# Kernel optimization log

Measured on AMD Instinct MI355X. Metric: run time of the kernel, lower is better.

The kernel has to match this reference:

```python
import jax, jax.numpy as jnp
import numpy as np

N_HEADS = 12
ROPE_THETA = 10000.0


def _rope(x):
    # x: [B, L, N, D]; interleaved (lucidrains rotary_embedding_torch style) rotation over full D
    B, L, N, D = x.shape
    inv_freq = 1.0 / (ROPE_THETA ** (jnp.arange(0, D, 2, dtype=jnp.float32) / D))  # [D/2]
    freqs = jnp.arange(L, dtype=jnp.float32)[:, None] * inv_freq                    # [L, D/2]
    cos = jnp.repeat(jnp.cos(freqs), 2, axis=-1)[None, :, None, :].astype(x.dtype)  # [1,L,1,D]
    sin = jnp.repeat(jnp.sin(freqs), 2, axis=-1)[None, :, None, :].astype(x.dtype)
    x1 = x[..., 0::2]
    x2 = x[..., 1::2]
    x_rot = jnp.stack([-x2, x1], axis=-1).reshape(x.shape)  # rotate_half, interleaved pairs
    return x * cos + x_rot * sin


def setup_inputs() -> dict:
    key = jax.random.key(0)
    ks = jax.random.split(key, 7)
    B, L, dm = 8, 1024, 768
    x = jax.random.normal(ks[0], (B, L, dm), jnp.float32)
    mask = jax.random.randint(ks[1], (B, L), 0, 2, jnp.int32)          # 1 = keep, 0 = pad
    pos_bias = jax.random.normal(ks[2], (N_HEADS, L, L), jnp.float32) * 0.1
    qkv_w = jax.random.normal(ks[3], (3 * dm, dm), jnp.float32) * 0.02
    qkv_b = jax.random.normal(ks[4], (3 * dm,), jnp.float32) * 0.02
    out_w = jax.random.normal(ks[5], (dm, dm), jnp.float32) * 0.02
    out_b = jax.random.normal(ks[6], (dm,), jnp.float32) * 0.02
    return {"x": x, "pos_bias": pos_bias, "qkv_w": qkv_w, "qkv_b": qkv_b,
            "out_w": out_w, "out_b": out_b, "mask": mask}


def reference(x, pos_bias, qkv_w, qkv_b, out_w, out_b, mask):
    B, L, dm = x.shape
    N = N_HEADS
    D = dm // N
    # QKV projection (torch Linear: y = x @ W.T + b), chunk(3, -1)
    qkv = x @ qkv_w.T + qkv_b                                   # [B, L, 3*dm]
    q, k, v = [a.reshape(B, L, N, D) for a in jnp.split(qkv, 3, axis=-1)]
    q = _rope(q)
    k = _rope(k)
    # scores [B, N, Lq, Lk]
    scores = jnp.einsum('bqnd,bknd->bnqk', q, k) / jnp.sqrt(jnp.asarray(D, x.dtype))
    # mask_to_bias: (mask - 1) with negatives -> -inf, shape [B, 1, 1, L]
    mask_bias = jnp.where(mask > 0, 0.0, -jnp.inf).astype(x.dtype)[:, None, None, :]
    bias = pos_bias[None].astype(x.dtype) + mask_bias           # [B, N, L, L]
    attn = jax.nn.softmax(scores + bias, axis=-1)               # dropout = 0 (eval)
    o = jnp.einsum('bnqk,bknd->bqnd', attn, v).reshape(B, L, dm)
    return o @ out_w.T + out_b
```

## Files before the change

### kernel.cpp

```cpp
#include <hip/hip_runtime.h>

#define DEVINL __device__ __forceinline__

using bf16x8 = __attribute__((ext_vector_type(8))) short;
using f32x4  = __attribute__((ext_vector_type(4))) float;

constexpr int Bb = 8, Ls = 1024, DM = 768, NH = 12, DH = 64;
constexpr int QKV = 3 * DM;

DEVINL unsigned short f2bf(float f) {
    union { float f; unsigned u; } v; v.f = f;
    unsigned r = v.u + 0x7FFFu + ((v.u >> 16) & 1u);
    return (unsigned short)(r >> 16);
}
DEVINL float bf2f(unsigned short h) {
    union { unsigned u; float f; } v; v.u = ((unsigned)h) << 16; return v.f;
}

DEVINL void gload_lds16(const void* g, void* l) {
    __builtin_amdgcn_global_load_lds((const __attribute__((address_space(1))) void*)g,
                                     (__attribute__((address_space(3))) void*)l, 16, 0, 0);
}

__global__ void prep_kernel(const float* __restrict__ x, const float* __restrict__ wq,
                            const float* __restrict__ wo,
                            unsigned short* __restrict__ xb, unsigned short* __restrict__ wqb,
                            unsigned short* __restrict__ wob, float* __restrict__ tab) {
    const int X4 = Bb * Ls * DM / 4, W4 = QKV * DM / 4, O4 = DM * DM / 4, TB = Ls * DH;
    const int total = X4 + W4 + O4 + TB;
    for (int idx = blockIdx.x * blockDim.x + threadIdx.x; idx < total;
         idx += gridDim.x * blockDim.x) {
        if (idx < X4 + W4 + O4) {
            const float4* s; unsigned short* d; int i;
            if (idx < X4)            { s = (const float4*)x;  d = xb;  i = idx; }
            else if (idx < X4 + W4)  { s = (const float4*)wq; d = wqb; i = idx - X4; }
            else                     { s = (const float4*)wo; d = wob; i = idx - X4 - W4; }
            float4 v = s[i];
            ushort4 o;
            o.x = f2bf(v.x); o.y = f2bf(v.y); o.z = f2bf(v.z); o.w = f2bf(v.w);
            ((ushort4*)d)[i] = o;
        } else {
            int r = idx - (X4 + W4 + O4);
            int l = r >> 6, c = r & 63, i = c & 31;
            float freq = powf(10000.0f, -(float)i / 32.0f);
            float ang = (float)l * freq;
            tab[l * 64 + c] = (c < 32) ? cosf(ang) : sinf(ang);
        }
    }
}

template <int OUT_BF16>
__global__ __launch_bounds__(256) void gemm_nt(const unsigned short* __restrict__ A,
                                               const unsigned short* __restrict__ Bw,
                                               const float* __restrict__ bias,
                                               void* __restrict__ Cout,
                                               int M, int Nn, int K) {
    __shared__ unsigned short As[128 * 32];
    __shared__ unsigned short Bs[128 * 32];
    const int tid = threadIdx.x, lane = tid & 63, w = tid >> 6;
    const int bm = blockIdx.x * 128, bn = blockIdx.y * 128;
    const int wm = w >> 1, wn = w & 1;
    const int col = lane & 15, q4 = lane >> 4;
    f32x4 acc[4][4] = {};
    for (int kb = 0; kb < K; kb += 32) {
#pragma unroll
        for (int i = 0; i < 2; ++i) {
            int c0 = w * 128 + i * 64;
            int p = c0 + lane;
            int row = p >> 2;
            int kc = (p & 3) ^ (row & 3);
            gload_lds16(A + (size_t)(bm + row) * K + kb + kc * 8, &As[c0 * 8]);
            gload_lds16(Bw + (size_t)(bn + row) * K + kb + kc * 8, &Bs[c0 * 8]);
        }
        __syncthreads();
        bf16x8 af[4], bfr[4];
#pragma unroll
        for (int t = 0; t < 4; ++t) {
            int ra = wm * 64 + t * 16 + col;
            int rb = wn * 64 + t * 16 + col;
            af[t]  = *(const bf16x8*)&As[(ra * 32 + q4 * 8) ^ ((ra & 3) << 3)];
            bfr[t] = *(const bf16x8*)&Bs[(rb * 32 + q4 * 8) ^ ((rb & 3) << 3)];
        }
#pragma unroll
        for (int t = 0; t < 4; ++t)
#pragma unroll
            for (int u = 0; u < 4; ++u)
                acc[t][u] = __builtin_amdgcn_mfma_f32_16x16x32_bf16(af[t], bfr[u], acc[t][u], 0, 0, 0);
        __syncthreads();
    }
#pragma unroll
    for (int t = 0; t < 4; ++t) {
        int grow_base = bm + wm * 64 + t * 16 + q4 * 4;
#pragma unroll
        for (int u = 0; u < 4; ++u) {
            int gcol = bn + wn * 64 + u * 16 + col;
            float bv = bias[gcol];
#pragma unroll
            for (int r = 0; r < 4; ++r) {
                float vv = acc[t][u][r] + bv;
                if (OUT_BF16)
                    ((unsigned short*)Cout)[(size_t)(grow_base + r) * Nn + gcol] = f2bf(vv);
                else
                    ((float*)Cout)[(size_t)(grow_base + r) * Nn + gcol] = vv;
            }
        }
    }
}

__global__ void rope_qk(const unsigned short* __restrict__ qkvb, const float* __restrict__ tab,
                        unsigned short* __restrict__ qs, unsigned short* __restrict__ ks) {
    const int b = blockIdx.z, n = blockIdx.y;
    const int idx = blockIdx.x * blockDim.x + threadIdx.x;
    const int l = idx >> 3, d8 = idx & 7;
    const unsigned short* src = qkvb + (size_t)(b * Ls + l) * QKV + n * DH + d8 * 8;
    float4 cs = *(const float4*)&tab[l * 64 + d8 * 4];
    float4 sn = *(const float4*)&tab[l * 64 + 32 + d8 * 4];
    float cv[4] = {cs.x, cs.y, cs.z, cs.w};
    float sv[4] = {sn.x, sn.y, sn.z, sn.w};
    size_t dsto = ((size_t)(b * NH + n) * Ls + l) * DH + d8 * 8;
    {
        bf16x8 qv = *(const bf16x8*)src;
        bf16x8 ov;
#pragma unroll
        for (int j = 0; j < 4; ++j) {
            float x1 = bf2f((unsigned short)qv[2 * j]), x2 = bf2f((unsigned short)qv[2 * j + 1]);
            ov[2 * j]     = (short)f2bf((x1 * cv[j] - x2 * sv[j]) * 0.125f);
            ov[2 * j + 1] = (short)f2bf((x2 * cv[j] + x1 * sv[j]) * 0.125f);
        }
        *(bf16x8*)(qs + dsto) = ov;
    }
    {
        bf16x8 kv = *(const bf16x8*)(src + DM);
        bf16x8 ov;
#pragma unroll
        for (int j = 0; j < 4; ++j) {
            float x1 = bf2f((unsigned short)kv[2 * j]), x2 = bf2f((unsigned short)kv[2 * j + 1]);
            ov[2 * j]     = (short)f2bf(x1 * cv[j] - x2 * sv[j]);
            ov[2 * j + 1] = (short)f2bf(x2 * cv[j] + x1 * sv[j]);
        }
        *(bf16x8*)(ks + dsto) = ov;
    }
}

__global__ void vtrans(const unsigned short* __restrict__ qkvb, unsigned short* __restrict__ vt) {
    __shared__ unsigned short vsh[64][72];
    const int b = blockIdx.z, n = blockIdx.y, lt = blockIdx.x;
    const int tid = threadIdx.x;
#pragma unroll
    for (int i = 0; i < 2; ++i) {
        int c = tid + i * 256;
        int lrow = c >> 3, d8 = c & 7;
        *(bf16x8*)&vsh[lrow][d8 * 8] =
            *(const bf16x8*)(qkvb + (size_t)(b * Ls + lt * 64 + lrow) * QKV + 2 * DM + n * DH + d8 * 8);
    }
    __syncthreads();
#pragma unroll
    for (int i = 0; i < 2; ++i) {
        int c = tid + i * 256;
        int d = c >> 3, l8 = c & 7;
        bf16x8 v;
#pragma unroll
        for (int j = 0; j < 8; ++j) v[j] = (short)vsh[l8 * 8 + j][d];
        *(bf16x8*)(vt + ((size_t)(b * NH + n) * DH + d) * Ls + lt * 64 + l8 * 8) = v;
    }
}

__global__ __launch_bounds__(256) void attn_kernel(const unsigned short* __restrict__ qs,
                                                   const unsigned short* __restrict__ ks,
                                                   const unsigned short* __restrict__ vt,
                                                   const float* __restrict__ posb,
                                                   const int* __restrict__ mask,
                                                   unsigned short* __restrict__ ob) {
    __shared__ unsigned short Ksh[64 * 64];
    __shared__ unsigned short Vsh[64 * 64];
    __shared__ unsigned short Psh[4][16 * 64];
    __shared__ float maskb[Ls];
    const int b = blockIdx.z, n = blockIdx.y, qt = blockIdx.x;
    const int tid = threadIdx.x, lane = tid & 63, w = tid >> 6;
    const int col = lane & 15, q4 = lane >> 4;
    for (int i = tid; i < Ls; i += 256)
        maskb[i] = (mask[b * Ls + i] > 0) ? 0.0f : -1e30f;
    const unsigned short* qbn = qs + (size_t)(b * NH + n) * Ls * DH;
    const unsigned short* kbn = ks + (size_t)(b * NH + n) * Ls * DH;
    const unsigned short* vbn = vt + (size_t)(b * NH + n) * DH * Ls;
    const float* pb = posb + (size_t)n * Ls * Ls;
    bf16x8 qf[2];
#pragma unroll
    for (int j = 0; j < 2; ++j)
        qf[j] = *(const bf16x8*)(qbn + (size_t)(qt * 64 + w * 16 + col) * DH + q4 * 8 + j * 32);
    const int qrow_c = w * 16 + q4 * 4;
    float mrun[4], lrun[4];
    f32x4 oacc[4];
#pragma unroll
    for (int r = 0; r < 4; ++r) { mrun[r] = -1e30f; lrun[r] = 0.f; }
#pragma unroll
    for (int t = 0; t < 4; ++t) oacc[t] = f32x4{0.f, 0.f, 0.f, 0.f};

    for (int kt = 0; kt < Ls / 64; ++kt) {
#pragma unroll
        for (int i = 0; i < 2; ++i) {
            int c0 = w * 128 + i * 64;
            int p = c0 + lane;
            int row = p >> 3, cin = (p & 7) ^ (row & 7);
            gload_lds16(kbn + (size_t)(kt * 64 + row) * DH + cin * 8, &Ksh[c0 * 8]);
            gload_lds16(vbn + (size_t)row * Ls + kt * 64 + cin * 8, &Vsh[c0 * 8]);
        }
        __syncthreads();
        f32x4 s[4];
#pragma unroll
        for (int t = 0; t < 4; ++t) {
            s[t] = f32x4{0.f, 0.f, 0.f, 0.f};
            int krow = t * 16 + col;
#pragma unroll
            for (int j = 0; j < 2; ++j) {
                bf16x8 kf = *(const bf16x8*)&Ksh[(krow * 64 + q4 * 8 + j * 32) ^ ((krow & 7) << 3)];
                s[t] = __builtin_amdgcn_mfma_f32_16x16x32_bf16(qf[j], kf, s[t], 0, 0, 0);
            }
        }
        float svv[4][4];
#pragma unroll
        for (int t = 0; t < 4; ++t) {
            int kg = kt * 64 + t * 16 + col;
            float mb = maskb[kg];
#pragma unroll
            for (int r = 0; r < 4; ++r) {
                int qg = qt * 64 + qrow_c + r;
                svv[t][r] = s[t][r] + pb[(size_t)qg * Ls + kg] + mb;
            }
        }
        float pm[4], al[4];
#pragma unroll
        for (int r = 0; r < 4; ++r) {
            pm[r] = fmaxf(fmaxf(svv[0][r], svv[1][r]), fmaxf(svv[2][r], svv[3][r]));
#pragma unroll
            for (int msk = 1; msk < 16; msk <<= 1)
                pm[r] = fmaxf(pm[r], __shfl_xor(pm[r], msk));
            float mn = fmaxf(mrun[r], pm[r]);
            al[r] = __expf(mrun[r] - mn);
            mrun[r] = mn;
        }
        float p[4][4], ps[4];
#pragma unroll
        for (int r = 0; r < 4; ++r) ps[r] = 0.f;
#pragma unroll
        for (int t = 0; t < 4; ++t)
#pragma unroll
            for (int r = 0; r < 4; ++r) {
                p[t][r] = __expf(svv[t][r] - mrun[r]);
                ps[r] += p[t][r];
            }
#pragma unroll
        for (int r = 0; r < 4; ++r) {
#pragma unroll
            for (int msk = 1; msk < 16; msk <<= 1)
                ps[r] += __shfl_xor(ps[r], msk);
            lrun[r] = lrun[r] * al[r] + ps[r];
        }
#pragma unroll
        for (int t = 0; t < 4; ++t)
#pragma unroll
            for (int r = 0; r < 4; ++r) oacc[t][r] *= al[r];
        unsigned short* pw = Psh[w];
#pragma unroll
        for (int t = 0; t < 4; ++t)
#pragma unroll
            for (int r = 0; r < 4; ++r) {
                int row = q4 * 4 + r;
                pw[(row * 64 + t * 16 + col) ^ ((row & 7) << 3)] = f2bf(p[t][r]);
            }
#pragma unroll
        for (int ot = 0; ot < 4; ++ot) {
            int vrow = ot * 16 + col;
#pragma unroll
            for (int j = 0; j < 2; ++j) {
                bf16x8 pa = *(const bf16x8*)&pw[(col * 64 + q4 * 8 + j * 32) ^ ((col & 7) << 3)];
                bf16x8 vb = *(const bf16x8*)&Vsh[(vrow * 64 + q4 * 8 + j * 32) ^ ((vrow & 7) << 3)];
                oacc[ot] = __builtin_amdgcn_mfma_f32_16x16x32_bf16(pa, vb, oacc[ot], 0, 0, 0);
            }
        }
        __syncthreads();
    }
#pragma unroll
    for (int r = 0; r < 4; ++r) {
        int lg = qt * 64 + qrow_c + r;
        float inv = 1.0f / lrun[r];
#pragma unroll
        for (int ot = 0; ot < 4; ++ot)
            ob[(size_t)(b * Ls + lg) * DM + n * DH + ot * 16 + col] = f2bf(oacc[ot][r] * inv);
    }
}

extern "C" void kernel_launch(void* const* d_in, const int* in_sizes, int n_in,
                              void* d_out, int out_size, void* d_ws, size_t ws_size,
                              hipStream_t stream) {
    const float* x     = (const float*)d_in[0];
    const float* posb  = (const float*)d_in[1];
    const float* qkv_w = (const float*)d_in[2];
    const float* qkv_b = (const float*)d_in[3];
    const float* out_w = (const float*)d_in[4];
    const float* out_b = (const float*)d_in[5];
    const int*   mask  = (const int*)d_in[6];
    float* out = (float*)d_out;

    char* wp = (char*)d_ws;
    auto alloc = [&](size_t bytes) {
        char* p = wp;
        wp += (bytes + 255) & ~(size_t)255;
        return p;
    };
    unsigned short* xb   = (unsigned short*)alloc((size_t)Bb * Ls * DM * 2);
    unsigned short* wqb  = (unsigned short*)alloc((size_t)QKV * DM * 2);
    unsigned short* wob  = (unsigned short*)alloc((size_t)DM * DM * 2);
    float*          tab  = (float*)alloc((size_t)Ls * DH * 4);
    unsigned short* qkvb = (unsigned short*)alloc((size_t)Bb * Ls * QKV * 2);
    unsigned short* qsb  = (unsigned short*)alloc((size_t)Bb * NH * Ls * DH * 2);
    unsigned short* ksb  = (unsigned short*)alloc((size_t)Bb * NH * Ls * DH * 2);
    unsigned short* vtb  = (unsigned short*)alloc((size_t)Bb * NH * DH * Ls * 2);
    unsigned short* obb  = (unsigned short*)alloc((size_t)Bb * Ls * DM * 2);

    prep_kernel<<<dim3(2048), dim3(256), 0, stream>>>(x, qkv_w, out_w, xb, wqb, wob, tab);
    gemm_nt<1><<<dim3(64, 18), dim3(256), 0, stream>>>(xb, wqb, qkv_b, (void*)qkvb, Bb * Ls, QKV, DM);
    rope_qk<<<dim3(32, NH, Bb), dim3(256), 0, stream>>>(qkvb, tab, qsb, ksb);
    vtrans<<<dim3(16, NH, Bb), dim3(256), 0, stream>>>(qkvb, vtb);
    attn_kernel<<<dim3(16, NH, Bb), dim3(256), 0, stream>>>(qsb, ksb, vtb, posb, mask, obb);
    gemm_nt<0><<<dim3(64, 6), dim3(256), 0, stream>>>(obb, wob, out_b, (void*)out, Bb * Ls, DM, DM);
}
```

Measured before the change: 296.2 us.

## Drop online softmax max tracking; precompute exp(pos_bias) in bf16 and stage in LDS

Precomputes exp(pos_bias) as bf16 in the prep kernel and folds log2(e) into the Q scale. The attention kernel then forms probabilities as exp2(score+mask)*exp_bias, with no running max, rescaling or per-tile shuffle reductions, and sums the row once at the end. Bias tiles are loaded into LDS asynchronously instead of being read as scattered fp32 global loads. The grid is reordered so blocks that share a head's bias tile run together. It risks overflow without max subtraction and loses some precision from the bf16 bias, and it adds a 24 MB elementwise pass in prep.

```diff
diff --git a/kernel.cpp b/kernel.cpp
--- a/kernel.cpp
+++ b/kernel.cpp
@@ -23,11 +23,13 @@
 }
 
 __global__ void prep_kernel(const float* __restrict__ x, const float* __restrict__ wq,
-                            const float* __restrict__ wo,
+                            const float* __restrict__ wo, const float* __restrict__ pbias,
                             unsigned short* __restrict__ xb, unsigned short* __restrict__ wqb,
-                            unsigned short* __restrict__ wob, float* __restrict__ tab) {
-    const int X4 = Bb * Ls * DM / 4, W4 = QKV * DM / 4, O4 = DM * DM / 4, TB = Ls * DH;
-    const int total = X4 + W4 + O4 + TB;
+                            unsigned short* __restrict__ wob, unsigned short* __restrict__ ebb,
+                            float* __restrict__ tab) {
+    const int X4 = Bb * Ls * DM / 4, W4 = QKV * DM / 4, O4 = DM * DM / 4;
+    const int E4 = NH * Ls * Ls / 4, TB = Ls * DH;
+    const int total = X4 + W4 + O4 + E4 + TB;
     for (int idx = blockIdx.x * blockDim.x + threadIdx.x; idx < total;
          idx += gridDim.x * blockDim.x) {
         if (idx < X4 + W4 + O4) {
@@ -39,8 +41,15 @@
             ushort4 o;
             o.x = f2bf(v.x); o.y = f2bf(v.y); o.z = f2bf(v.z); o.w = f2bf(v.w);
             ((ushort4*)d)[i] = o;
+        } else if (idx < X4 + W4 + O4 + E4) {
+            int i = idx - (X4 + W4 + O4);
+            float4 v = ((const float4*)pbias)[i];
+            ushort4 o;
+            o.x = f2bf(__expf(v.x)); o.y = f2bf(__expf(v.y));
+            o.z = f2bf(__expf(v.z)); o.w = f2bf(__expf(v.w));
+            ((ushort4*)ebb)[i] = o;
         } else {
-            int r = idx - (X4 + W4 + O4);
+            int r = idx - (X4 + W4 + O4 + E4);
             int l = r >> 6, c = r & 63, i = c & 31;
             float freq = powf(10000.0f, -(float)i / 32.0f);
             float ang = (float)l * freq;
@@ -112,6 +121,7 @@
     const int b = blockIdx.z, n = blockIdx.y;
     const int idx = blockIdx.x * blockDim.x + threadIdx.x;
     const int l = idx >> 3, d8 = idx & 7;
+    const float QSCL = 0.125f * 1.44269504089f;
     const unsigned short* src = qkvb + (size_t)(b * Ls + l) * QKV + n * DH + d8 * 8;
     float4 cs = *(const float4*)&tab[l * 64 + d8 * 4];
     float4 sn = *(const float4*)&tab[l * 64 + 32 + d8 * 4];
@@ -124,8 +134,8 @@
 #pragma unroll
         for (int j = 0; j < 4; ++j) {
             float x1 = bf2f((unsigned short)qv[2 * j]), x2 = bf2f((unsigned short)qv[2 * j + 1]);
-            ov[2 * j]     = (short)f2bf((x1 * cv[j] - x2 * sv[j]) * 0.125f);
-            ov[2 * j + 1] = (short)f2bf((x2 * cv[j] + x1 * sv[j]) * 0.125f);
+            ov[2 * j]     = (short)f2bf((x1 * cv[j] - x2 * sv[j]) * QSCL);
+            ov[2 * j + 1] = (short)f2bf((x2 * cv[j] + x1 * sv[j]) * QSCL);
         }
         *(bf16x8*)(qs + dsto) = ov;
     }
@@ -168,14 +178,15 @@
 __global__ __launch_bounds__(256) void attn_kernel(const unsigned short* __restrict__ qs,
                                                    const unsigned short* __restrict__ ks,
                                                    const unsigned short* __restrict__ vt,
-                                                   const float* __restrict__ posb,
+                                                   const unsigned short* __restrict__ ebb,
                                                    const int* __restrict__ mask,
                                                    unsigned short* __restrict__ ob) {
     __shared__ unsigned short Ksh[64 * 64];
     __shared__ unsigned short Vsh[64 * 64];
+    __shared__ unsigned short EBsh[64 * 64];
     __shared__ unsigned short Psh[4][16 * 64];
     __shared__ float maskb[Ls];
-    const int b = blockIdx.z, n = blockIdx.y, qt = blockIdx.x;
+    const int b = blockIdx.x, n = blockIdx.y, qt = blockIdx.z;
     const int tid = threadIdx.x, lane = tid & 63, w = tid >> 6;
     const int col = lane & 15, q4 = lane >> 4;
     for (int i = tid; i < Ls; i += 256)
@@ -183,16 +194,14 @@
     const unsigned short* qbn = qs + (size_t)(b * NH + n) * Ls * DH;
     const unsigned short* kbn = ks + (size_t)(b * NH + n) * Ls * DH;
     const unsigned short* vbn = vt + (size_t)(b * NH + n) * DH * Ls;
-    const float* pb = posb + (size_t)n * Ls * Ls;
+    const unsigned short* ebn = ebb + (size_t)n * Ls * Ls;
     bf16x8 qf[2];
 #pragma unroll
     for (int j = 0; j < 2; ++j)
         qf[j] = *(const bf16x8*)(qbn + (size_t)(qt * 64 + w * 16 + col) * DH + q4 * 8 + j * 32);
     const int qrow_c = w * 16 + q4 * 4;
-    float mrun[4], lrun[4];
+    float psum[4] = {0.f, 0.f, 0.f, 0.f};
     f32x4 oacc[4];
-#pragma unroll
-    for (int r = 0; r < 4; ++r) { mrun[r] = -1e30f; lrun[r] = 0.f; }
 #pragma unroll
     for (int t = 0; t < 4; ++t) oacc[t] = f32x4{0.f, 0.f, 0.f, 0.f};
 
@@ -204,6 +213,7 @@
             int row = p >> 3, cin = (p & 7) ^ (row & 7);
             gload_lds16(kbn + (size_t)(kt * 64 + row) * DH + cin * 8, &Ksh[c0 * 8]);
             gload_lds16(vbn + (size_t)row * Ls + kt * 64 + cin * 8, &Vsh[c0 * 8]);
+            gload_lds16(ebn + (size_t)(qt * 64 + row) * Ls + kt * 64 + cin * 8, &EBsh[c0 * 8]);
         }
         __syncthreads();
         f32x4 s[4];
@@ -217,49 +227,22 @@
                 s[t] = __builtin_amdgcn_mfma_f32_16x16x32_bf16(qf[j], kf, s[t], 0, 0, 0);
             }
         }
-        float svv[4][4];
+        float p[4][4];
 #pragma unroll
         for (int t = 0; t < 4; ++t) {
             int kg = kt * 64 + t * 16 + col;
-            float mb = maskb[kg];
+            float ma = maskb[kg];
+            int chunk = t * 2 + (col >> 3);
 #pragma unroll
             for (int r = 0; r < 4; ++r) {
-                int qg = qt * 64 + qrow_c + r;
-                svv[t][r] = s[t][r] + pb[(size_t)qg * Ls + kg] + mb;
-            }
-        }
-        float pm[4], al[4];
-#pragma unroll
-        for (int r = 0; r < 4; ++r) {
-            pm[r] = fmaxf(fmaxf(svv[0][r], svv[1][r]), fmaxf(svv[2][r], svv[3][r]));
-#pragma unroll
-            for (int msk = 1; msk < 16; msk <<= 1)
-                pm[r] = fmaxf(pm[r], __shfl_xor(pm[r], msk));
-            float mn = fmaxf(mrun[r], pm[r]);
-            al[r] = __expf(mrun[r] - mn);
-            mrun[r] = mn;
-        }
-        float p[4][4], ps[4];
-#pragma unroll
-        for (int r = 0; r < 4; ++r) ps[r] = 0.f;
-#pragma unroll
-        for (int t = 0; t < 4; ++t)
-#pragma unroll
-            for (int r = 0; r < 4; ++r) {
-                p[t][r] = __expf(svv[t][r] - mrun[r]);
-                ps[r] += p[t][r];
-            }
-#pragma unroll
-        for (int r = 0; r < 4; ++r) {
-#pragma unroll
-            for (int msk = 1; msk < 16; msk <<= 1)
-                ps[r] += __shfl_xor(ps[r], msk);
-            lrun[r] = lrun[r] * al[r] + ps[r];
-        }
-#pragma unroll
-        for (int t = 0; t < 4; ++t)
-#pragma unroll
-            for (int r = 0; r < 4; ++r) oacc[t][r] *= al[r];
+                int rowl = qrow_c + r;
+                int bo = rowl * 128 + (((chunk ^ (rowl & 7)) << 4)) + ((col & 7) << 1);
+                float ebf = bf2f(*(const unsigned short*)((const char*)EBsh + bo));
+                float pv = exp2f(s[t][r] + ma) * ebf;
+                p[t][r] = pv;
+                psum[r] += pv;
+            }
+        }
         unsigned short* pw = Psh[w];
 #pragma unroll
         for (int t = 0; t < 4; ++t)
@@ -281,9 +264,14 @@
         __syncthreads();
     }
 #pragma unroll
+    for (int r = 0; r < 4; ++r)
+#pragma unroll
+        for (int msk = 1; msk < 16; msk <<= 1)
+            psum[r] += __shfl_xor(psum[r], msk);
+#pragma unroll
     for (int r = 0; r < 4; ++r) {
         int lg = qt * 64 + qrow_c + r;
-        float inv = 1.0f / lrun[r];
+        float inv = 1.0f / psum[r];
 #pragma unroll
         for (int ot = 0; ot < 4; ++ot)
             ob[(size_t)(b * Ls + lg) * DM + n * DH + ot * 16 + col] = f2bf(oacc[ot][r] * inv);
@@ -311,6 +299,7 @@
     unsigned short* xb   = (unsigned short*)alloc((size_t)Bb * Ls * DM * 2);
     unsigned short* wqb  = (unsigned short*)alloc((size_t)QKV * DM * 2);
     unsigned short* wob  = (unsigned short*)alloc((size_t)DM * DM * 2);
+    unsigned short* ebb  = (unsigned short*)alloc((size_t)NH * Ls * Ls * 2);
     float*          tab  = (float*)alloc((size_t)Ls * DH * 4);
     unsigned short* qkvb = (unsigned short*)alloc((size_t)Bb * Ls * QKV * 2);
     unsigned short* qsb  = (unsigned short*)alloc((size_t)Bb * NH * Ls * DH * 2);
@@ -318,10 +307,10 @@
     unsigned short* vtb  = (unsigned short*)alloc((size_t)Bb * NH * DH * Ls * 2);
     unsigned short* obb  = (unsigned short*)alloc((size_t)Bb * Ls * DM * 2);
 
-    prep_kernel<<<dim3(2048), dim3(256), 0, stream>>>(x, qkv_w, out_w, xb, wqb, wob, tab);
+    prep_kernel<<<dim3(2048), dim3(256), 0, stream>>>(x, qkv_w, out_w, posb, xb, wqb, wob, ebb, tab);
     gemm_nt<1><<<dim3(64, 18), dim3(256), 0, stream>>>(xb, wqb, qkv_b, (void*)qkvb, Bb * Ls, QKV, DM);
     rope_qk<<<dim3(32, NH, Bb), dim3(256), 0, stream>>>(qkvb, tab, qsb, ksb);
     vtrans<<<dim3(16, NH, Bb), dim3(256), 0, stream>>>(qkvb, vtb);
-    attn_kernel<<<dim3(16, NH, Bb), dim3(256), 0, stream>>>(qsb, ksb, vtb, posb, mask, obb);
+    attn_kernel<<<dim3(Bb, NH, 16), dim3(256), 0, stream>>>(qsb, ksb, vtb, ebb, mask, obb);
     gemm_nt<0><<<dim3(64, 6), dim3(256), 0, stream>>>(obb, wob, out_b, (void*)out, Bb * Ls, DM, DM);
 }
```

After: 294.2 us. About the same (-0.7%).
